# Performance work log

Hardware: AMD Instinct MI355X
Metric: run time of the kernel (lower is better)

Reference implementation:

```python
import jax, jax.numpy as jnp
import numpy as np

MARGIN = 0.3
BIG = 9999999.0


def setup_inputs() -> dict:
    key = jax.random.key(0)
    k1, k2, k3 = jax.random.split(key, 3)
    N, D, D2, NUM_IDS = 8192, 1024, 512, 512
    emb = jax.random.normal(k1, (N, D), dtype=jnp.float32)
    clot_feats_s = jax.random.normal(k2, (N, D2), dtype=jnp.float32)
    label = jax.random.randint(k3, (N,), 0, NUM_IDS, dtype=jnp.int64)
    return {"emb": emb, "label": label, "clot_feats_s": clot_feats_s}


def _margin_ranking_loss(x1, x2, y, margin):
    # torch MarginRankingLoss: mean(max(0, -y*(x1-x2)+margin))
    return jnp.mean(jnp.maximum(0.0, -y * (x1 - x2) + margin))


def reference(emb, label, clot_feats_s):
    N = emb.shape[0]
    # euclidean_dist(emb, emb): [N,N]
    sq = jnp.sum(emb * emb, axis=1)
    dist = sq[:, None] + sq[None, :] - 2.0 * (emb @ emb.T)
    dist = jnp.sqrt(jnp.clip(dist, 1e-12, None))
    # cosine similarity of clot_feats_s with itself: [N,N]
    nrm = jnp.sqrt(jnp.sum(clot_feats_s * clot_feats_s, axis=1))
    cos = (clot_feats_s @ clot_feats_s.T) / (nrm[:, None] * nrm[None, :])
    # same-identity mask
    sim = (label[:, None] == label[None, :]).astype(dist.dtype)
    # batch-hard: top-2 positives (largest masked distance), hardest negative (smallest)
    pos_vals, pos_idx = jax.lax.top_k(dist - BIG * (1.0 - sim), 2)
    dist_ap1, dist_ap2 = pos_vals[:, 0], pos_vals[:, 1]
    neg_mat = dist + BIG * sim
    hard_n_idx = jnp.argmin(neg_mat, axis=1)
    dist_an = jnp.min(neg_mat, axis=1)
    rows = jnp.arange(N)
    # per-row gathers into cosine-sim matrix (detached in original)
    alpha1 = jax.lax.stop_gradient(cos[rows, pos_idx[:, 0]])
    alpha2 = jax.lax.stop_gradient(cos[rows, pos_idx[:, 1]])
    # (alphan gathered in original but unused in the loss)
    y11 = jnp.where(alpha1 < alpha2, -1.0, 1.0)
    y11_m = jnp.where(alpha1 == alpha2, 0.0, 1.0)
    loss11 = _margin_ranking_loss(
        dist_ap2 * y11_m,
        dist_ap1 * y11_m + MARGIN * (alpha1 - alpha2 - y11),
        y11, MARGIN)
    dist_ap1_m = dist_ap1 + MARGIN * (alpha1 - 1.0)
    loss13 = _margin_ranking_loss(dist_an, dist_ap1_m, 1.0, MARGIN)
    loss = 0.1 * loss11 + loss13
    prec = jnp.mean((dist_an > dist_ap1_m).astype(jnp.float32))
    return loss, prec
```

## Files before the change

### kernel.cpp

```cpp
#include <hip/hip_runtime.h>
#include <stdint.h>

#define NR 8192
#define DE 1024
#define DC 512
#define BIGF 9999999.0f
#define MARG 0.3f
#define NEGI -3.0e38f
#define POSI 3.0e38f
#define CAP 64

typedef __attribute__((ext_vector_type(8))) short bf16x8;
typedef __attribute__((ext_vector_type(4))) float f32x4;

typedef __attribute__((address_space(3))) unsigned int lds_u32;
typedef const __attribute__((address_space(1))) unsigned int glb_u32;

static __device__ __forceinline__ void ld_g2l16(const void* g, void* l) {
    __builtin_amdgcn_global_load_lds((glb_u32*)g, (lds_u32*)l, 16, 0, 0);
}

static __device__ __forceinline__ unsigned short f2bf(float x) {
    unsigned u = __float_as_uint(x);
    unsigned r = u + 0x7FFFu + ((u >> 16) & 1u);
    return (unsigned short)(r >> 16);
}

static __device__ __forceinline__ float b2f(short u) {
    return __uint_as_float(((unsigned)(unsigned short)u) << 16);
}

__global__ __launch_bounds__(256) void k_prep_emb(const float* __restrict__ emb,
                                                  const int* __restrict__ label,
                                                  short* __restrict__ embb,
                                                  float* __restrict__ sq,
                                                  int* __restrict__ cnt,
                                                  unsigned* __restrict__ mnA) {
    int w = threadIdx.x >> 6, lane = threadIdx.x & 63;
    int row = blockIdx.x * 4 + w;
    const float4* src = (const float4*)(emb + (size_t)row * DE);
    ushort4* dst = (ushort4*)(embb + (size_t)row * DE);
    float s = 0.f;
#pragma unroll
    for (int c = 0; c < 4; ++c) {
        float4 v = src[c * 64 + lane];
        s += v.x * v.x + v.y * v.y + v.z * v.z + v.w * v.w;
        ushort4 b;
        b.x = f2bf(v.x); b.y = f2bf(v.y); b.z = f2bf(v.z); b.w = f2bf(v.w);
        dst[c * 64 + lane] = b;
    }
    for (int m = 1; m < 64; m <<= 1) s += __shfl_xor(s, m);
    if (lane == 0) {
        sq[row] = s;
        atomicAdd(&cnt[label[row]], 1);
        mnA[row] = 0xFFFFFFFFu;
    }
}

__global__ __launch_bounds__(256) void k_fill(const int* __restrict__ cnt,
                                              const int* __restrict__ label,
                                              int* __restrict__ clsOff,
                                              int* __restrict__ fill,
                                              int* __restrict__ list,
                                              int* __restrict__ mIdx) {
    __shared__ int s[512];
    int t = threadIdx.x;
    s[t] = cnt[t];
    s[t + 256] = cnt[t + 256];
    __syncthreads();
    for (int d = 1; d < 512; d <<= 1) {
        int v0 = (t >= d) ? s[t - d] : 0;
        int v1 = s[t + 256 - d];
        __syncthreads();
        s[t] += v0;
        s[t + 256] += v1;
        __syncthreads();
    }
    if (blockIdx.x == 0) {
        clsOff[t] = s[t] - cnt[t];
        clsOff[t + 256] = s[t + 256] - cnt[t + 256];
    }
    int i = blockIdx.x * 256 + t;
    int l = label[i];
    int p = atomicAdd(&fill[l], 1);
    list[s[l] - cnt[l] + p] = i;
    mIdx[i] = p;
}

__global__ __launch_bounds__(256, 3) void k_main(const short* __restrict__ embb,
                                                 const float* __restrict__ sq,
                                                 const int* __restrict__ label,
                                                 const int* __restrict__ mIdx,
                                                 unsigned* __restrict__ mnA,
                                                 float* __restrict__ posmat) {
    const int b = blockIdx.x;
    int r = (int)((129.0f - sqrtf(16641.0f - 8.0f * (float)b)) * 0.5f);
    if (r < 0) r = 0;
    if (r > 63) r = 63;
    while (r > 0 && 64 * r - (r * (r - 1)) / 2 > b) --r;
    while (64 * (r + 1) - ((r + 1) * r) / 2 <= b) ++r;
    const int c = r + (b - (64 * r - (r * (r - 1)) / 2));
    const int i0 = r * 128, j0 = c * 128;

    __shared__ __align__(16) short As[128 * 64];
    __shared__ __align__(16) short Bs[128 * 64];

    const int tid = threadIdx.x;
    const int lane = tid & 63;
    const int w = tid >> 6;
    const int wr = w >> 1, wc = w & 1;
    const int q = lane >> 4, l15 = lane & 15;

    const int g = (tid & 7) ^ ((tid >> 3) & 7);
    const short* gA = embb + (size_t)(i0 + (tid >> 3)) * DE + g * 8;
    const short* gB = embb + (size_t)(j0 + (tid >> 3)) * DE + g * 8;

    const int swz = l15 & 7;

    auto stage = [&](int koff) {
#pragma unroll
        for (int n = 0; n < 4; ++n) {
            ld_g2l16(gA + (size_t)n * 32 * DE + koff, &As[n * 2048 + tid * 8]);
            ld_g2l16(gB + (size_t)n * 32 * DE + koff, &Bs[n * 2048 + tid * 8]);
        }
    };

    stage(0);

    f32x4 acc[4][4];
#pragma unroll
    for (int mi = 0; mi < 4; ++mi)
#pragma unroll
        for (int ni = 0; ni < 4; ++ni) acc[mi][ni] = (f32x4){0.f, 0.f, 0.f, 0.f};

    for (int ks = 0; ks < 16; ++ks) {
        __syncthreads();
        bf16x8 af[2][4], bfr[2][4];
#pragma unroll
        for (int kk = 0; kk < 2; ++kk) {
            const int kc = ((kk * 4 + q) ^ swz) * 8;
#pragma unroll
            for (int mi = 0; mi < 4; ++mi)
                af[kk][mi] = *(const bf16x8*)&As[(wr * 64 + mi * 16 + l15) * 64 + kc];
#pragma unroll
            for (int ni = 0; ni < 4; ++ni)
                bfr[kk][ni] = *(const bf16x8*)&Bs[(wc * 64 + ni * 16 + l15) * 64 + kc];
        }
#pragma unroll
        for (int kk = 0; kk < 2; ++kk)
#pragma unroll
            for (int mi = 0; mi < 4; ++mi)
#pragma unroll
                for (int ni = 0; ni < 4; ++ni)
                    acc[mi][ni] = __builtin_amdgcn_mfma_f32_16x16x32_bf16(af[kk][mi], bfr[kk][ni], acc[mi][ni], 0, 0, 0);
        __syncthreads();
        if (ks < 15) stage((ks + 1) * 64);
    }

    const int rb = i0 + wr * 64, cb = j0 + wc * 64;
    float sqj[4]; int lbj[4]; float cmn[4];
#pragma unroll
    for (int ni = 0; ni < 4; ++ni) {
        int cg = cb + ni * 16 + l15;
        sqj[ni] = sq[cg]; lbj[ni] = label[cg]; cmn[ni] = POSI;
    }
#pragma unroll
    for (int mi = 0; mi < 4; ++mi) {
        float rm[4] = {POSI, POSI, POSI, POSI};
        float sqi[4]; int lbi[4];
#pragma unroll
        for (int rr = 0; rr < 4; ++rr) {
            int rg = rb + mi * 16 + q * 4 + rr;
            sqi[rr] = sq[rg]; lbi[rr] = label[rg];
        }
#pragma unroll
        for (int ni = 0; ni < 4; ++ni)
#pragma unroll
            for (int rr = 0; rr < 4; ++rr) {
                float d2 = fmaf(-2.0f, acc[mi][ni][rr], sqi[rr] + sqj[ni]);
                d2 = fmaxf(d2, 1e-12f);
                if (lbi[rr] == lbj[ni]) {
                    int gi = rb + mi * 16 + q * 4 + rr;
                    int gj = cb + ni * 16 + l15;
                    int a = mIdx[gi], bb = mIdx[gj];
                    if (a < CAP && bb < CAP) {
                        float* pm = posmat + (size_t)lbi[rr] * CAP * CAP;
                        pm[a * CAP + bb] = d2;
                        pm[bb * CAP + a] = d2;
                    }
                }
                float dn = (lbi[rr] == lbj[ni]) ? POSI : d2;
                rm[rr] = fminf(rm[rr], dn);
                cmn[ni] = fminf(cmn[ni], dn);
            }
#pragma unroll
        for (int rr = 0; rr < 4; ++rr) {
            float v = rm[rr];
            v = fminf(v, __shfl_xor(v, 1));
            v = fminf(v, __shfl_xor(v, 2));
            v = fminf(v, __shfl_xor(v, 4));
            v = fminf(v, __shfl_xor(v, 8));
            if (l15 == 0) atomicMin(&mnA[rb + mi * 16 + q * 4 + rr], __float_as_uint(v));
        }
    }
#pragma unroll
    for (int ni = 0; ni < 4; ++ni) {
        float v = cmn[ni];
        v = fminf(v, __shfl_xor(v, 16));
        v = fminf(v, __shfl_xor(v, 32));
        if (q == 0) atomicMin(&mnA[cb + ni * 16 + l15], __float_as_uint(v));
    }
}

__global__ __launch_bounds__(256) void k_pos(const short* __restrict__ embb,
                                             const float* __restrict__ sq,
                                             const float* __restrict__ clot,
                                             const int* __restrict__ label,
                                             const int* __restrict__ cnt,
                                             const int* __restrict__ clsOff,
                                             const int* __restrict__ clsList,
                                             const int* __restrict__ mIdx,
                                             const float* __restrict__ posmat,
                                             const unsigned* __restrict__ mnA,
                                             float* __restrict__ ap1, float* __restrict__ ap2,
                                             float* __restrict__ an,
                                             float* __restrict__ alpha1, float* __restrict__ alpha2) {
    int wid = threadIdx.x >> 6, lane = threadIdx.x & 63;
    int row = blockIdx.x * 4 + wid;
    int lb = label[row];
    int cc = cnt[lb], off = clsOff[lb];
    float sqiv = sq[row];

    float v1 = NEGI, v2 = NEGI;
    int i1 = 0, i2 = 0;
    auto upd = [&](float d2, int j) {
        bool t1 = (d2 > v1) || (d2 == v1 && j < i1);
        bool t2 = (d2 > v2) || (d2 == v2 && j < i2);
        v2 = t1 ? v1 : (t2 ? d2 : v2);
        i2 = t1 ? i1 : (t2 ? j : i2);
        v1 = t1 ? d2 : v1;
        i1 = t1 ? j : i1;
    };

    if (cc <= CAP) {
        const int self = mIdx[row];
        if (lane < cc) {
            float d2 = (lane == self) ? 1e-12f
                                      : posmat[((size_t)lb * CAP + self) * CAP + lane];
            upd(d2, clsList[off + lane]);
        }
        for (int d = 1; d < 64; d <<= 1) {
            float o1 = __shfl_xor(v1, d), o2 = __shfl_xor(v2, d);
            int oi1 = __shfl_xor(i1, d), oi2 = __shfl_xor(i2, d);
            upd(o1, oi1);
            upd(o2, oi2);
        }
    } else {
        const bf16x8* rp = (const bf16x8*)(embb + (size_t)row * DE + lane * 16);
        bf16x8 ra = rp[0], rb = rp[1];
        float rf[16];
#pragma unroll
        for (int t = 0; t < 8; ++t) { rf[t] = b2f(ra[t]); rf[8 + t] = b2f(rb[t]); }
        for (int m = 0; m < cc; ++m) {
            int j = clsList[off + m];
            float d2;
            if (j == row) {
                d2 = 1e-12f;
            } else {
                const bf16x8* jp = (const bf16x8*)(embb + (size_t)j * DE + lane * 16);
                bf16x8 ja = jp[0], jb = jp[1];
                float s = 0.f;
#pragma unroll
                for (int t = 0; t < 8; ++t) s = fmaf(rf[t], b2f(ja[t]), s);
#pragma unroll
                for (int t = 0; t < 8; ++t) s = fmaf(rf[8 + t], b2f(jb[t]), s);
                for (int mm = 1; mm < 64; mm <<= 1) s += __shfl_xor(s, mm);
                d2 = fmaxf(fmaf(-2.0f, s, sqiv + sq[j]), 1e-12f);
            }
            upd(d2, j);
        }
    }

    float a1 = sqrtf(v1);
    int j1 = i1;
    float a2v; int j2;
    if (cc >= 2) {
        a2v = sqrtf(v2);
        j2 = i2;
    } else {
        float kv = NEGI; int ki = 0;
        for (int cr = lane; cr < NR; cr += 64) {
            if (label[cr] == lb) continue;
            float s = 0.f;
            const short* crow = embb + (size_t)cr * DE;
            const short* rrow = embb + (size_t)row * DE;
            for (int t = 0; t < DE; ++t) s = fmaf(b2f(rrow[t]), b2f(crow[t]), s);
            float d2c = fmaxf(fmaf(-2.0f, s, sqiv + sq[cr]), 1e-12f);
            bool tk = (d2c > kv) || (d2c == kv && cr < ki);
            kv = tk ? d2c : kv; ki = tk ? cr : ki;
        }
        for (int mm = 1; mm < 64; mm <<= 1) {
            float ov = __shfl_xor(kv, mm); int oi = __shfl_xor(ki, mm);
            bool tk = (ov > kv) || (ov == kv && oi < ki);
            kv = tk ? ov : kv; ki = tk ? oi : ki;
        }
        a2v = sqrtf(kv) - BIGF;
        j2 = ki;
    }

    const float4* c4 = (const float4*)clot;
    float s1 = 0.f, s2 = 0.f, n0 = 0.f, n1 = 0.f, n2 = 0.f;
    for (int t = lane; t < DC / 4; t += 64) {
        float4 a = c4[(size_t)row * (DC / 4) + t];
        float4 b1 = c4[(size_t)j1 * (DC / 4) + t];
        float4 b2 = c4[(size_t)j2 * (DC / 4) + t];
        s1 += a.x * b1.x + a.y * b1.y + a.z * b1.z + a.w * b1.w;
        s2 += a.x * b2.x + a.y * b2.y + a.z * b2.z + a.w * b2.w;
        n0 += a.x * a.x + a.y * a.y + a.z * a.z + a.w * a.w;
        n1 += b1.x * b1.x + b1.y * b1.y + b1.z * b1.z + b1.w * b1.w;
        n2 += b2.x * b2.x + b2.y * b2.y + b2.z * b2.z + b2.w * b2.w;
    }
    for (int mm = 1; mm < 64; mm <<= 1) {
        s1 += __shfl_xor(s1, mm); s2 += __shfl_xor(s2, mm);
        n0 += __shfl_xor(n0, mm); n1 += __shfl_xor(n1, mm); n2 += __shfl_xor(n2, mm);
    }
    if (lane == 0) {
        ap1[row] = a1; ap2[row] = a2v;
        an[row] = sqrtf(__uint_as_float(mnA[row]));
        alpha1[row] = s1 / (sqrtf(n0) * sqrtf(n1));
        alpha2[row] = s2 / (sqrtf(n0) * sqrtf(n2));
    }
}

__global__ __launch_bounds__(256) void k_final(const float* __restrict__ ap1, const float* __restrict__ ap2,
                                               const float* __restrict__ an,
                                               const float* __restrict__ alpha1, const float* __restrict__ alpha2,
                                               float* __restrict__ out) {
    int tid = threadIdx.x;
    float sl11 = 0.f, sl13 = 0.f, sp = 0.f;
    for (int row = tid; row < NR; row += 256) {
        float a1 = alpha1[row], a2 = alpha2[row];
        float dap1 = ap1[row], dap2 = ap2[row], dan = an[row];
        float y = (a1 < a2) ? -1.f : 1.f;
        float ym = (a1 == a2) ? 0.f : 1.f;
        float x1 = dap2 * ym;
        float x2 = dap1 * ym + MARG * (a1 - a2 - y);
        sl11 += fmaxf(0.f, -y * (x1 - x2) + MARG);
        float ap1m = dap1 + MARG * (a1 - 1.f);
        sl13 += fmaxf(0.f, -(dan - ap1m) + MARG);
        sp += (dan > ap1m) ? 1.f : 0.f;
    }
    for (int m = 1; m < 64; m <<= 1) {
        sl11 += __shfl_xor(sl11, m);
        sl13 += __shfl_xor(sl13, m);
        sp += __shfl_xor(sp, m);
    }
    __shared__ float r11[4], r13[4], rp[4];
    if ((tid & 63) == 0) { r11[tid >> 6] = sl11; r13[tid >> 6] = sl13; rp[tid >> 6] = sp; }
    __syncthreads();
    if (tid == 0) {
        float t11 = r11[0] + r11[1] + r11[2] + r11[3];
        float t13 = r13[0] + r13[1] + r13[2] + r13[3];
        float tp = rp[0] + rp[1] + rp[2] + rp[3];
        out[0] = 0.1f * (t11 / (float)NR) + t13 / (float)NR;
        out[1] = tp / (float)NR;
    }
}

extern "C" void kernel_launch(void* const* d_in, const int* in_sizes, int n_in,
                              void* d_out, int out_size, void* d_ws, size_t ws_size,
                              hipStream_t stream) {
    const float* emb = (const float*)d_in[0];
    const int* label = (const int*)d_in[1];
    const float* clot = (const float*)d_in[2];
    float* out = (float*)d_out;

    char* ws = (char*)d_ws;
    size_t off = 0;
    auto alloc = [&](size_t bytes) -> char* {
        char* p = ws + off;
        off = (off + bytes + 255) & ~(size_t)255;
        return p;
    };
    short*    embb = (short*)alloc((size_t)NR * DE * 2);
    float*    pmat = (float*)alloc((size_t)512 * CAP * CAP * 4);
    float*    sq   = (float*)alloc(NR * 4);
    int*      cnt  = (int*)alloc(512 * 4);
    int*      fill = (int*)alloc(512 * 4);
    int*      cOff = (int*)alloc(512 * 4);
    int*      list = (int*)alloc(NR * 4);
    int*      mIdx = (int*)alloc(NR * 4);
    unsigned* mnA  = (unsigned*)alloc((size_t)NR * 4);
    float*    ap1  = (float*)alloc(NR * 4);
    float*    ap2  = (float*)alloc(NR * 4);
    float*    an   = (float*)alloc(NR * 4);
    float*    al1  = (float*)alloc(NR * 4);
    float*    al2  = (float*)alloc(NR * 4);

    hipMemsetAsync(cnt, 0, 2 * 512 * 4, stream);

    k_prep_emb<<<dim3(NR / 4), dim3(256), 0, stream>>>(emb, label, embb, sq, cnt, mnA);
    k_fill<<<dim3(NR / 256), dim3(256), 0, stream>>>(cnt, label, cOff, fill, list, mIdx);
    k_main<<<dim3(2080), dim3(256), 0, stream>>>(embb, sq, label, mIdx, mnA, pmat);
    k_pos<<<dim3(NR / 4), dim3(256), 0, stream>>>(embb, sq, clot, label, cnt, cOff, list,
                                                  mIdx, pmat, mnA, ap1, ap2, an, al1, al2);
    k_final<<<dim3(1), dim3(256), 0, stream>>>(ap1, ap2, an, al1, al2, out);
}
```

Before: 219.1 us.

## Double-buffer LDS tiles with K=32 stages and one barrier per step

```diff
diff --git a/kernel.cpp b/kernel.cpp
--- a/kernel.cpp
+++ b/kernel.cpp
@@ -102,8 +102,8 @@
     const int c = r + (b - (64 * r - (r * (r - 1)) / 2));
     const int i0 = r * 128, j0 = c * 128;
 
-    __shared__ __align__(16) short As[128 * 64];
-    __shared__ __align__(16) short Bs[128 * 64];
+    __shared__ __align__(16) short As[2][128 * 32];
+    __shared__ __align__(16) short Bs[2][128 * 32];
 
     const int tid = threadIdx.x;
     const int lane = tid & 63;
@@ -111,21 +111,21 @@
     const int wr = w >> 1, wc = w & 1;
     const int q = lane >> 4, l15 = lane & 15;
 
-    const int g = (tid & 7) ^ ((tid >> 3) & 7);
-    const short* gA = embb + (size_t)(i0 + (tid >> 3)) * DE + g * 8;
-    const short* gB = embb + (size_t)(j0 + (tid >> 3)) * DE + g * 8;
-
-    const int swz = l15 & 7;
-
-    auto stage = [&](int koff) {
-#pragma unroll
-        for (int n = 0; n < 4; ++n) {
-            ld_g2l16(gA + (size_t)n * 32 * DE + koff, &As[n * 2048 + tid * 8]);
-            ld_g2l16(gB + (size_t)n * 32 * DE + koff, &Bs[n * 2048 + tid * 8]);
-        }
+    const int g = (tid & 3) ^ ((tid >> 3) & 3);
+    const short* gA = embb + (size_t)(i0 + (tid >> 2)) * DE + g * 8;
+    const short* gB = embb + (size_t)(j0 + (tid >> 2)) * DE + g * 8;
+
+    const int pxor = q ^ ((l15 >> 1) & 3);
+
+    auto stage = [&](int koff, int p) {
+        ld_g2l16(gA + koff, &As[p][(size_t)tid * 8]);
+        ld_g2l16(gA + (size_t)64 * DE + koff, &As[p][(size_t)(tid + 256) * 8]);
+        ld_g2l16(gB + koff, &Bs[p][(size_t)tid * 8]);
+        ld_g2l16(gB + (size_t)64 * DE + koff, &Bs[p][(size_t)(tid + 256) * 8]);
     };
 
-    stage(0);
+    stage(0, 0);
+    int p = 0;
 
     f32x4 acc[4][4];
 #pragma unroll
@@ -133,28 +133,22 @@
 #pragma unroll
         for (int ni = 0; ni < 4; ++ni) acc[mi][ni] = (f32x4){0.f, 0.f, 0.f, 0.f};
 
-    for (int ks = 0; ks < 16; ++ks) {
+    for (int ks = 0; ks < 32; ++ks) {
         __syncthreads();
-        bf16x8 af[2][4], bfr[2][4];
-#pragma unroll
-        for (int kk = 0; kk < 2; ++kk) {
-            const int kc = ((kk * 4 + q) ^ swz) * 8;
-#pragma unroll
-            for (int mi = 0; mi < 4; ++mi)
-                af[kk][mi] = *(const bf16x8*)&As[(wr * 64 + mi * 16 + l15) * 64 + kc];
+        if (ks < 31) stage((ks + 1) * 32, p ^ 1);
+        bf16x8 af[4], bfr[4];
+#pragma unroll
+        for (int mi = 0; mi < 4; ++mi)
+            af[mi] = *(const bf16x8*)&As[p][(wr * 64 + mi * 16 + l15) * 32 + pxor * 8];
+#pragma unroll
+        for (int ni = 0; ni < 4; ++ni)
+            bfr[ni] = *(const bf16x8*)&Bs[p][(wc * 64 + ni * 16 + l15) * 32 + pxor * 8];
+#pragma unroll
+        for (int mi = 0; mi < 4; ++mi)
 #pragma unroll
             for (int ni = 0; ni < 4; ++ni)
-                bfr[kk][ni] = *(const bf16x8*)&Bs[(wc * 64 + ni * 16 + l15) * 64 + kc];
-        }
-#pragma unroll
-        for (int kk = 0; kk < 2; ++kk)
-#pragma unroll
-            for (int mi = 0; mi < 4; ++mi)
-#pragma unroll
-                for (int ni = 0; ni < 4; ++ni)
-                    acc[mi][ni] = __builtin_amdgcn_mfma_f32_16x16x32_bf16(af[kk][mi], bfr[kk][ni], acc[mi][ni], 0, 0, 0);
-        __syncthreads();
-        if (ks < 15) stage((ks + 1) * 64);
+                acc[mi][ni] = __builtin_amdgcn_mfma_f32_16x16x32_bf16(af[mi], bfr[ni], acc[mi][ni], 0, 0, 0);
+        p ^= 1;
     }
 
     const int rb = i0 + wr * 64, cb = j0 + wc * 64;
```

Result: slower. 229.2 us (+4.6%).
